# Performance work log

Measured on AMD Instinct MI355X. Metric: run time of the kernel, lower is better.

## Reference

```python
import jax, jax.numpy as jnp
import numpy as np

HIDDEN = 1024
HEADS = 16
HEAD_DIM = HIDDEN // HEADS
B, S = 2, 2048


def setup_inputs() -> dict:
    key = jax.random.key(0)
    ks = jax.random.split(key, 9)
    sc = 1.0 / np.sqrt(HIDDEN)
    return {
        "hidden_state": jax.random.normal(ks[0], (B, S, HIDDEN), dtype=jnp.float32),
        "wq": jax.random.normal(ks[1], (HIDDEN, HIDDEN), dtype=jnp.float32) * sc,
        "bq": jax.random.normal(ks[2], (HIDDEN,), dtype=jnp.float32) * 0.01,
        "wk": jax.random.normal(ks[3], (HIDDEN, HIDDEN), dtype=jnp.float32) * sc,
        "bk": jax.random.normal(ks[4], (HIDDEN,), dtype=jnp.float32) * 0.01,
        "wv": jax.random.normal(ks[5], (HIDDEN, HIDDEN), dtype=jnp.float32) * sc,
        "bv": jax.random.normal(ks[6], (HIDDEN,), dtype=jnp.float32) * 0.01,
        "wo": jax.random.normal(ks[7], (HIDDEN, HIDDEN), dtype=jnp.float32) * sc,
        "bo": jax.random.normal(ks[8], (HIDDEN,), dtype=jnp.float32) * 0.01,
    }


def reference(hidden_state, wq, bq, wk, bk, wv, bv, wo, bo):
    b, s, _ = hidden_state.shape

    def split_head(x):  # [B,S,H*D] -> [B,H,S,D]
        return x.reshape(b, s, HEADS, HEAD_DIM).transpose(0, 2, 1, 3)

    q = split_head(hidden_state @ wq + bq)
    k = split_head(hidden_state @ wk + bk)
    v = split_head(hidden_state @ wv + bv)

    # NOTE: original scales by sqrt(hidden_size), NOT sqrt(head_dim)
    scale = 1.0 / jnp.sqrt(jnp.float32(HIDDEN))
    scores = jnp.einsum("bhqd,bhkd->bhqk", q, k) * scale  # [B,H,S,S]
    probs = jax.nn.softmax(scores, axis=-1)
    out = jnp.einsum("bhqk,bhkd->bhqd", probs, v)  # [B,H,S,D]

    # Faithful to source: transpose(-1,-2) then view (this is the original's
    # layout, which differs from the conventional transpose(1,2) merge)
    out = out.transpose(0, 1, 3, 2).reshape(b, -1, HEADS * HEAD_DIM)
    return out @ wo + bo
```

## Files before the change

### kernel.cpp

```cpp
#include <hip/hip_runtime.h>
#include <stdint.h>


typedef unsigned short u16;
typedef __bf16 bf16x8 __attribute__((ext_vector_type(8)));
typedef u16 u16x8 __attribute__((ext_vector_type(8)));
typedef u16 u16x4 __attribute__((ext_vector_type(4)));
typedef float f32x4 __attribute__((ext_vector_type(4)));

#define DEV static __device__ __forceinline__

DEV bf16x8 as_bf16x8(u16x8 u) { union { u16x8 u; bf16x8 b; } c; c.u = u; return c.b; }
DEV u16 f2bf(float f) {
  uint32_t u = __float_as_uint(f);
  u += 0x7fffu + ((u >> 16) & 1u);
  return (u16)(u >> 16);
}
#if __has_builtin(__builtin_amdgcn_exp2f)
DEV float ex2(float x) { return __builtin_amdgcn_exp2f(x); }
#else
DEV float ex2(float x) { return exp2f(x); }
#endif

DEV void gll16(const u16* g, u16* lds) {
  __builtin_amdgcn_global_load_lds((const __attribute__((address_space(1))) void*)g,
                                   (__attribute__((address_space(3))) void*)lds,
                                   16, 0, 0);
}

__global__ __launch_bounds__(256) void prep_kernel(
    const float* __restrict__ hid, const float* __restrict__ w0,
    const float* __restrict__ w1, const float* __restrict__ w2,
    const float* __restrict__ w3, u16* __restrict__ Ah,
    u16* __restrict__ Wt) {
  __shared__ __align__(16) float T[64][68];
  int bid = blockIdx.x, t = threadIdx.x;
  if (bid < 2048) {
    int i = (bid * 256 + t) * 8;
    f32x4 a = *(const f32x4*)&hid[i];
    f32x4 b = *(const f32x4*)&hid[i + 4];
    u16x8 o;
#pragma unroll
    for (int j = 0; j < 4; ++j) { o[j] = f2bf(a[j]); o[j + 4] = f2bf(b[j]); }
    *(u16x8*)&Ah[i] = o;
    return;
  }
  int tb = bid - 2048;
  int z = tb >> 8, rem = tb & 255;
  const float* W = (z == 0) ? w0 : (z == 1) ? w1 : (z == 2) ? w2 : w3;
  u16* O = Wt + (size_t)z * 1024 * 1024;
  int r0 = (rem >> 4) * 64, c0 = (rem & 15) * 64;
  int i = t >> 2, js = (t & 3) * 16;
#pragma unroll
  for (int jj = 0; jj < 16; jj += 4)
    *(f32x4*)&T[i][js + jj] = *(const f32x4*)&W[(size_t)(r0 + i) * 1024 + c0 + js + jj];
  __syncthreads();
#pragma unroll
  for (int seg = 0; seg < 2; ++seg) {
    u16x8 v;
#pragma unroll
    for (int jj = 0; jj < 8; ++jj) v[jj] = f2bf(T[js + seg * 8 + jj][i]);
    *(u16x8*)&O[(size_t)(c0 + i) * 1024 + r0 + js + seg * 8] = v;
  }
}

DEV void gemm_body(const u16* __restrict__ A, const u16* __restrict__ Bt,
                   const float* __restrict__ bias, u16* __restrict__ C,
                   int mode, float scale) {
  __shared__ __align__(16) u16 As[128 * 32], Bs[128 * 32];
  int tid = threadIdx.x, lane = tid & 63, w = tid >> 6;
  int quad = lane >> 4, l15 = lane & 15;
  int m0 = blockIdx.x * 128, n0 = blockIdx.y * 128;
  int wm = w >> 1, wn = w & 1;
  f32x4 acc[4][4] = {};

  for (int k0 = 0; k0 < 1024; k0 += 32) {
    __syncthreads();
#pragma unroll
    for (int i = 0; i < 2; ++i) {
      int idx = i * 256 + w * 64 + lane;
      int row = idx >> 2, cs = idx & 3, c = cs ^ ((row >> 1) & 3);
      gll16(A + (size_t)(m0 + row) * 1024 + k0 + c * 8, &As[(i * 256 + w * 64) * 8]);
      gll16(Bt + (size_t)(n0 + row) * 1024 + k0 + c * 8, &Bs[(i * 256 + w * 64) * 8]);
    }
    __syncthreads();
    bf16x8 af[4], bfr[4];
#pragma unroll
    for (int mt = 0; mt < 4; ++mt) {
      int row = wm * 64 + mt * 16 + l15;
      af[mt] = as_bf16x8(*(const u16x8*)&As[row * 32 + (quad ^ ((row >> 1) & 3)) * 8]);
    }
#pragma unroll
    for (int nt = 0; nt < 4; ++nt) {
      int row = wn * 64 + nt * 16 + l15;
      bfr[nt] = as_bf16x8(*(const u16x8*)&Bs[row * 32 + (quad ^ ((row >> 1) & 3)) * 8]);
    }
#pragma unroll
    for (int mt = 0; mt < 4; ++mt)
#pragma unroll
      for (int nt = 0; nt < 4; ++nt)
        acc[mt][nt] = __builtin_amdgcn_mfma_f32_16x16x32_bf16(af[mt], bfr[nt], acc[mt][nt], 0, 0, 0);
  }

#pragma unroll
  for (int nt = 0; nt < 4; ++nt) {
    int n = n0 + wn * 64 + nt * 16 + l15;
    float bv = bias[n];
#pragma unroll
    for (int mt = 0; mt < 4; ++mt) {
      int mbase = m0 + wm * 64 + mt * 16 + quad * 4;
      if (mode == 2) {
        int b = mbase >> 11, s = mbase & 2047, h = n >> 6, d = n & 63;
        size_t base = (((size_t)(b * 16 + h)) * 64 + d) * 2048 + s;
        u16x4 pk;
#pragma unroll
        for (int r = 0; r < 4; ++r) pk[r] = f2bf((acc[mt][nt][r] + bv) * scale);
        *(u16x4*)&C[base] = pk;
      } else {
#pragma unroll
        for (int r = 0; r < 4; ++r) {
          int m = mbase + r;
          int b = m >> 11, s = m & 2047, h = n >> 6, d = n & 63;
          C[(((size_t)(b * 16 + h)) * 2048 + s) * 64 + d] =
              f2bf((acc[mt][nt][r] + bv) * scale);
        }
      }
    }
  }
}

__global__ __launch_bounds__(256) void qkv_gemm(
    const u16* __restrict__ A, const u16* __restrict__ Wt,
    const float* __restrict__ bq, const float* __restrict__ bk,
    const float* __restrict__ bv, u16* __restrict__ Qb, u16* __restrict__ Kb,
    u16* __restrict__ Vt) {
  int z = blockIdx.z;
  const u16* Bt = Wt + (size_t)z * 1024 * 1024;
  const float* bias = (z == 0) ? bq : (z == 1) ? bk : bv;
  u16* C = (z == 0) ? Qb : (z == 1) ? Kb : Vt;
  gemm_body(A, Bt, bias, C, (z == 2) ? 2 : 1, (z == 0) ? 0.045084220f : 1.0f);
}

__global__ __launch_bounds__(256) void out_gemm(
    const u16* __restrict__ A, const u16* __restrict__ Wt,
    const float* __restrict__ bo, float* __restrict__ C) {
  const u16* Bt = Wt + (size_t)3 * 1024 * 1024;
  __shared__ __align__(16) u16 As[64 * 32], Bs[128 * 32];
  int tid = threadIdx.x, lane = tid & 63, w = tid >> 6;
  int quad = lane >> 4, l15 = lane & 15;
  int m0 = blockIdx.x * 64, n0 = blockIdx.y * 128;
  f32x4 acc[4][2] = {};

  for (int k0 = 0; k0 < 1024; k0 += 32) {
    __syncthreads();
    {
      int idx = w * 64 + lane;
      int row = idx >> 2, cs = idx & 3, c = cs ^ ((row >> 1) & 3);
      gll16(A + (size_t)(m0 + row) * 1024 + k0 + c * 8, &As[(w * 64) * 8]);
#pragma unroll
      for (int i = 0; i < 2; ++i) {
        int bidx = i * 256 + w * 64 + lane;
        int brow = bidx >> 2, bcs = bidx & 3, bc = bcs ^ ((brow >> 1) & 3);
        gll16(Bt + (size_t)(n0 + brow) * 1024 + k0 + bc * 8,
              &Bs[(i * 256 + w * 64) * 8]);
      }
    }
    __syncthreads();
    bf16x8 af[4], bfr[2];
#pragma unroll
    for (int mt = 0; mt < 4; ++mt) {
      int row = mt * 16 + l15;
      af[mt] = as_bf16x8(*(const u16x8*)&As[row * 32 + (quad ^ ((row >> 1) & 3)) * 8]);
    }
#pragma unroll
    for (int nt = 0; nt < 2; ++nt) {
      int row = w * 32 + nt * 16 + l15;
      bfr[nt] = as_bf16x8(*(const u16x8*)&Bs[row * 32 + (quad ^ ((row >> 1) & 3)) * 8]);
    }
#pragma unroll
    for (int mt = 0; mt < 4; ++mt)
#pragma unroll
      for (int nt = 0; nt < 2; ++nt)
        acc[mt][nt] = __builtin_amdgcn_mfma_f32_16x16x32_bf16(af[mt], bfr[nt], acc[mt][nt], 0, 0, 0);
  }

#pragma unroll
  for (int nt = 0; nt < 2; ++nt) {
    int n = n0 + w * 32 + nt * 16 + l15;
    float bv = bo[n];
#pragma unroll
    for (int mt = 0; mt < 4; ++mt) {
      int mbase = m0 + mt * 16 + quad * 4;
#pragma unroll
      for (int r = 0; r < 4; ++r)
        C[(size_t)(mbase + r) * 1024 + n] = acc[mt][nt][r] + bv;
    }
  }
}

#define PSTR 80
__global__ __launch_bounds__(256, 2) void attn_kernel(
    const u16* __restrict__ Qb, const u16* __restrict__ Kb,
    const u16* __restrict__ Vtb, u16* __restrict__ Otb) {
  __shared__ __align__(16) u16 Ks[2][64 * PSTR], Vs[2][64 * PSTR];
  int tid = threadIdx.x, lane = tid & 63, w = tid >> 6;
  int quad = lane >> 4, l15 = lane & 15;
  int bh = blockIdx.x, q0 = blockIdx.y * 128;
  const size_t baseQK = (size_t)bh * 2048 * 64;

  bf16x8 bq[2][2];
#pragma unroll
  for (int g = 0; g < 2; ++g) {
    int qrow = q0 + w * 32 + g * 16 + l15;
#pragma unroll
    for (int ks = 0; ks < 2; ++ks)
      bq[g][ks] = as_bf16x8(*(const u16x8*)&Qb[baseQK + (size_t)qrow * 64 + (ks * 4 + quad) * 8]);
  }

  bf16x8 av1;
  {
    u16x8 o1;
#pragma unroll
    for (int j = 0; j < 8; ++j) o1[j] = 0x3F80;
    av1 = as_bf16x8(o1);
  }

  f32x4 o[2][4] = {};
  f32x4 l_acc[2] = {};
  const int km = ((l15 & 12) << 1) | (l15 & 3);
  const int srow = tid >> 3, scs = tid & 7;
  const int srow2 = 32 + srow;

  u16x8 tk[2], tv[2];
  tk[0] = *(const u16x8*)&Kb[baseQK + (size_t)srow * 64 + scs * 8];
  tk[1] = *(const u16x8*)&Kb[baseQK + (size_t)srow2 * 64 + scs * 8];
  tv[0] = *(const u16x8*)&Vtb[baseQK + (size_t)srow * 2048 + scs * 8];
  tv[1] = *(const u16x8*)&Vtb[baseQK + (size_t)srow2 * 2048 + scs * 8];
  *(u16x8*)&Ks[0][srow * PSTR + scs * 8] = tk[0];
  *(u16x8*)&Ks[0][srow2 * PSTR + scs * 8] = tk[1];
  *(u16x8*)&Vs[0][srow * PSTR + scs * 8] = tv[0];
  *(u16x8*)&Vs[0][srow2 * PSTR + scs * 8] = tv[1];
  __syncthreads();

  for (int kv = 0; kv < 32; ++kv) {
    int cur = kv & 1;
    if (kv < 31) {
      tk[0] = *(const u16x8*)&Kb[baseQK + (size_t)((kv + 1) * 64 + srow) * 64 + scs * 8];
      tk[1] = *(const u16x8*)&Kb[baseQK + (size_t)((kv + 1) * 64 + srow2) * 64 + scs * 8];
      tv[0] = *(const u16x8*)&Vtb[baseQK + (size_t)srow * 2048 + (kv + 1) * 64 + scs * 8];
      tv[1] = *(const u16x8*)&Vtb[baseQK + (size_t)srow2 * 2048 + (kv + 1) * 64 + scs * 8];
    }

    f32x4 scA[2][2] = {}, scB[2][2] = {};
    __builtin_amdgcn_s_setprio(1);
#pragma unroll
    for (int ks = 0; ks < 2; ++ks)
#pragma unroll
      for (int mtg = 0; mtg < 2; ++mtg) {
        bf16x8 akA = as_bf16x8(*(const u16x8*)&Ks[cur][(mtg * 32 + km) * PSTR + (ks * 4 + quad) * 8]);
        bf16x8 akB = as_bf16x8(*(const u16x8*)&Ks[cur][(mtg * 32 + km + 4) * PSTR + (ks * 4 + quad) * 8]);
#pragma unroll
        for (int g = 0; g < 2; ++g) {
          scA[g][mtg] = __builtin_amdgcn_mfma_f32_16x16x32_bf16(akA, bq[g][ks], scA[g][mtg], 0, 0, 0);
          scB[g][mtg] = __builtin_amdgcn_mfma_f32_16x16x32_bf16(akB, bq[g][ks], scB[g][mtg], 0, 0, 0);
        }
      }
    __builtin_amdgcn_s_setprio(0);

    bf16x8 bp[2][2];
#pragma unroll
    for (int g = 0; g < 2; ++g)
#pragma unroll
      for (int mtg = 0; mtg < 2; ++mtg) {
        float pA0 = ex2(scA[g][mtg][0]), pA1 = ex2(scA[g][mtg][1]);
        float pA2 = ex2(scA[g][mtg][2]), pA3 = ex2(scA[g][mtg][3]);
        float pB0 = ex2(scB[g][mtg][0]), pB1 = ex2(scB[g][mtg][1]);
        float pB2 = ex2(scB[g][mtg][2]), pB3 = ex2(scB[g][mtg][3]);
        bp[g][mtg] = (bf16x8){(__bf16)pA0, (__bf16)pA1, (__bf16)pA2, (__bf16)pA3,
                              (__bf16)pB0, (__bf16)pB1, (__bf16)pB2, (__bf16)pB3};
        l_acc[g] = __builtin_amdgcn_mfma_f32_16x16x32_bf16(av1, bp[g][mtg], l_acc[g], 0, 0, 0);
      }

    __builtin_amdgcn_s_setprio(1);
#pragma unroll
    for (int mtg = 0; mtg < 2; ++mtg)
#pragma unroll
      for (int dt = 0; dt < 4; ++dt) {
        bf16x8 av = as_bf16x8(*(const u16x8*)&Vs[cur][(dt * 16 + l15) * PSTR + (mtg * 4 + quad) * 8]);
#pragma unroll
        for (int g = 0; g < 2; ++g)
          o[g][dt] = __builtin_amdgcn_mfma_f32_16x16x32_bf16(av, bp[g][mtg], o[g][dt], 0, 0, 0);
      }
    __builtin_amdgcn_s_setprio(0);

    if (kv < 31) {
      int nb = cur ^ 1;
      *(u16x8*)&Ks[nb][srow * PSTR + scs * 8] = tk[0];
      *(u16x8*)&Ks[nb][srow2 * PSTR + scs * 8] = tk[1];
      *(u16x8*)&Vs[nb][srow * PSTR + scs * 8] = tv[0];
      *(u16x8*)&Vs[nb][srow2 * PSTR + scs * 8] = tv[1];
    }
    __syncthreads();
  }

#pragma unroll
  for (int g = 0; g < 2; ++g) {
    float inv = 1.0f / l_acc[g][0];
#pragma unroll
    for (int dt = 0; dt < 4; ++dt)
#pragma unroll
      for (int r = 0; r < 4; ++r) {
        int d = dt * 16 + quad * 4 + r;
        Otb[(size_t)bh * 64 * 2048 + (size_t)d * 2048 + q0 + w * 32 + g * 16 + l15] =
            f2bf(o[g][dt][r] * inv);
      }
  }
}

extern "C" void kernel_launch(void* const* d_in, const int* in_sizes, int n_in,
                              void* d_out, int out_size, void* d_ws, size_t ws_size,
                              hipStream_t stream) {
  const float* hid = (const float*)d_in[0];
  const float* wq = (const float*)d_in[1];
  const float* bq = (const float*)d_in[2];
  const float* wk = (const float*)d_in[3];
  const float* bk = (const float*)d_in[4];
  const float* wv = (const float*)d_in[5];
  const float* bv = (const float*)d_in[6];
  const float* wo = (const float*)d_in[7];
  const float* bo = (const float*)d_in[8];

  u16* ws = (u16*)d_ws;
  const size_t MB2 = (size_t)1024 * 1024;
  u16* Wt  = ws;
  u16* Ah  = ws + 4 * MB2;
  u16* Qb  = ws + 8 * MB2;
  u16* Kb  = ws + 12 * MB2;
  u16* Vtb = ws + 16 * MB2;
  u16* Otb = Ah;

  prep_kernel<<<3072, 256, 0, stream>>>(hid, wq, wk, wv, wo, Ah, Wt);
  qkv_gemm<<<dim3(32, 8, 3), 256, 0, stream>>>(Ah, Wt, bq, bk, bv, Qb, Kb, Vtb);
  attn_kernel<<<dim3(32, 16), 256, 0, stream>>>(Qb, Kb, Vtb, Otb);
  out_gemm<<<dim3(64, 8), 256, 0, stream>>>(Otb, Wt, bo, (float*)d_out);
}
```

Before: 181.8 us.

## Split attention KV range across two blocks and add a combine kernel

Splits each attention block's 32 KV tiles into two halves handled by separate blocks (grid z=2). Each half writes its unnormalized partial output in bf16 plus its row sums, and a new combine kernel adds the halves, normalizes and writes the transposed output. This doubles the number of workgroups from 512 to 1024 so more of the GPU's compute units have work. The change also drops LDS double buffering for a single buffer with two barriers per tile, and adds an XOR swizzle on K and a tighter V stride. The costs are an extra launch, extra global traffic for the partials, and an extra bf16 rounding of the partial outputs.

```diff
diff --git a/kernel.cpp b/kernel.cpp
--- a/kernel.cpp
+++ b/kernel.cpp
@@ -16,6 +16,7 @@
   u += 0x7fffu + ((u >> 16) & 1u);
   return (u16)(u >> 16);
 }
+DEV float bf2f(u16 u) { return __uint_as_float((uint32_t)u << 16); }
 #if __has_builtin(__builtin_amdgcn_exp2f)
 DEV float ex2(float x) { return __builtin_amdgcn_exp2f(x); }
 #else
@@ -198,15 +199,19 @@
   }
 }
 
-#define PSTR 80
+#define KSTR 80
+#define VSTR 72
 __global__ __launch_bounds__(256, 2) void attn_kernel(
     const u16* __restrict__ Qb, const u16* __restrict__ Kb,
-    const u16* __restrict__ Vtb, u16* __restrict__ Otb) {
-  __shared__ __align__(16) u16 Ks[2][64 * PSTR], Vs[2][64 * PSTR];
+    const u16* __restrict__ Vtb, u16* __restrict__ opart,
+    float* __restrict__ lpart) {
+  __shared__ __align__(16) u16 Ks[64 * KSTR], Vs[64 * VSTR];
   int tid = threadIdx.x, lane = tid & 63, w = tid >> 6;
   int quad = lane >> 4, l15 = lane & 15;
-  int bh = blockIdx.x, q0 = blockIdx.y * 128;
+  int bh = blockIdx.x, qb = blockIdx.y, z = blockIdx.z;
+  int q0 = qb * 128;
   const size_t baseQK = (size_t)bh * 2048 * 64;
+  const int kvbase = z * 16;
 
   bf16x8 bq[2][2];
 #pragma unroll
@@ -228,23 +233,26 @@
   f32x4 o[2][4] = {};
   f32x4 l_acc[2] = {};
   const int km = ((l15 & 12) << 1) | (l15 & 3);
+  const int swz = l15 >> 2;
   const int srow = tid >> 3, scs = tid & 7;
   const int srow2 = 32 + srow;
+  const int scw = scs ^ (srow >> 3);
 
   u16x8 tk[2], tv[2];
-  tk[0] = *(const u16x8*)&Kb[baseQK + (size_t)srow * 64 + scs * 8];
-  tk[1] = *(const u16x8*)&Kb[baseQK + (size_t)srow2 * 64 + scs * 8];
-  tv[0] = *(const u16x8*)&Vtb[baseQK + (size_t)srow * 2048 + scs * 8];
-  tv[1] = *(const u16x8*)&Vtb[baseQK + (size_t)srow2 * 2048 + scs * 8];
-  *(u16x8*)&Ks[0][srow * PSTR + scs * 8] = tk[0];
-  *(u16x8*)&Ks[0][srow2 * PSTR + scs * 8] = tk[1];
-  *(u16x8*)&Vs[0][srow * PSTR + scs * 8] = tv[0];
-  *(u16x8*)&Vs[0][srow2 * PSTR + scs * 8] = tv[1];
-  __syncthreads();
-
-  for (int kv = 0; kv < 32; ++kv) {
-    int cur = kv & 1;
-    if (kv < 31) {
+  tk[0] = *(const u16x8*)&Kb[baseQK + (size_t)(kvbase * 64 + srow) * 64 + scs * 8];
+  tk[1] = *(const u16x8*)&Kb[baseQK + (size_t)(kvbase * 64 + srow2) * 64 + scs * 8];
+  tv[0] = *(const u16x8*)&Vtb[baseQK + (size_t)srow * 2048 + kvbase * 64 + scs * 8];
+  tv[1] = *(const u16x8*)&Vtb[baseQK + (size_t)srow2 * 2048 + kvbase * 64 + scs * 8];
+
+  for (int kv = kvbase; kv < kvbase + 16; ++kv) {
+    __syncthreads();
+    *(u16x8*)&Ks[srow * KSTR + scw * 8] = tk[0];
+    *(u16x8*)&Ks[srow2 * KSTR + scw * 8] = tk[1];
+    *(u16x8*)&Vs[srow * VSTR + scs * 8] = tv[0];
+    *(u16x8*)&Vs[srow2 * VSTR + scs * 8] = tv[1];
+    __syncthreads();
+
+    if (kv < kvbase + 15) {
       tk[0] = *(const u16x8*)&Kb[baseQK + (size_t)((kv + 1) * 64 + srow) * 64 + scs * 8];
       tk[1] = *(const u16x8*)&Kb[baseQK + (size_t)((kv + 1) * 64 + srow2) * 64 + scs * 8];
       tv[0] = *(const u16x8*)&Vtb[baseQK + (size_t)srow * 2048 + (kv + 1) * 64 + scs * 8];
@@ -257,8 +265,9 @@
     for (int ks = 0; ks < 2; ++ks)
 #pragma unroll
       for (int mtg = 0; mtg < 2; ++mtg) {
-        bf16x8 akA = as_bf16x8(*(const u16x8*)&Ks[cur][(mtg * 32 + km) * PSTR + (ks * 4 + quad) * 8]);
-        bf16x8 akB = as_bf16x8(*(const u16x8*)&Ks[cur][(mtg * 32 + km + 4) * PSTR + (ks * 4 + quad) * 8]);
+        int ck = ((ks * 4 + quad) ^ swz) * 8;
+        bf16x8 akA = as_bf16x8(*(const u16x8*)&Ks[(mtg * 32 + km) * KSTR + ck]);
+        bf16x8 akB = as_bf16x8(*(const u16x8*)&Ks[(mtg * 32 + km + 4) * KSTR + ck]);
 #pragma unroll
         for (int g = 0; g < 2; ++g) {
           scA[g][mtg] = __builtin_amdgcn_mfma_f32_16x16x32_bf16(akA, bq[g][ks], scA[g][mtg], 0, 0, 0);
@@ -286,34 +295,67 @@
     for (int mtg = 0; mtg < 2; ++mtg)
 #pragma unroll
       for (int dt = 0; dt < 4; ++dt) {
-        bf16x8 av = as_bf16x8(*(const u16x8*)&Vs[cur][(dt * 16 + l15) * PSTR + (mtg * 4 + quad) * 8]);
+        bf16x8 av = as_bf16x8(*(const u16x8*)&Vs[(dt * 16 + l15) * VSTR + (mtg * 4 + quad) * 8]);
 #pragma unroll
         for (int g = 0; g < 2; ++g)
           o[g][dt] = __builtin_amdgcn_mfma_f32_16x16x32_bf16(av, bp[g][mtg], o[g][dt], 0, 0, 0);
       }
     __builtin_amdgcn_s_setprio(0);
-
-    if (kv < 31) {
-      int nb = cur ^ 1;
-      *(u16x8*)&Ks[nb][srow * PSTR + scs * 8] = tk[0];
-      *(u16x8*)&Ks[nb][srow2 * PSTR + scs * 8] = tk[1];
-      *(u16x8*)&Vs[nb][srow * PSTR + scs * 8] = tv[0];
-      *(u16x8*)&Vs[nb][srow2 * PSTR + scs * 8] = tv[1];
-    }
-    __syncthreads();
-  }
-
+  }
+
+  int pid = bh * 16 + qb;
+  u16* op = opart + (size_t)(pid * 2 + z) * 128 * 64;
+  float* lp = lpart + (size_t)(pid * 2 + z) * 128;
 #pragma unroll
   for (int g = 0; g < 2; ++g) {
-    float inv = 1.0f / l_acc[g][0];
-#pragma unroll
-    for (int dt = 0; dt < 4; ++dt)
-#pragma unroll
-      for (int r = 0; r < 4; ++r) {
-        int d = dt * 16 + quad * 4 + r;
-        Otb[(size_t)bh * 64 * 2048 + (size_t)d * 2048 + q0 + w * 32 + g * 16 + l15] =
-            f2bf(o[g][dt][r] * inv);
-      }
+    int q = w * 32 + g * 16 + l15;
+    if (quad == 0) lp[q] = l_acc[g][0];
+#pragma unroll
+    for (int dt = 0; dt < 4; ++dt) {
+      u16x4 pk;
+#pragma unroll
+      for (int r = 0; r < 4; ++r) pk[r] = f2bf(o[g][dt][r]);
+      *(u16x4*)&op[q * 64 + dt * 16 + quad * 4] = pk;
+    }
+  }
+}
+
+__global__ __launch_bounds__(256) void attn_combine(
+    const u16* __restrict__ opart, const float* __restrict__ lpart,
+    u16* __restrict__ Otb) {
+  __shared__ float So[128][65];
+  __shared__ float Sl[128];
+  int tid = threadIdx.x, pid = blockIdx.x;
+  int bh = pid >> 4, q0 = (pid & 15) * 128;
+  const u16* o0 = opart + (size_t)pid * 2 * 128 * 64;
+  const u16* o1 = o0 + 128 * 64;
+  const float* l0 = lpart + (size_t)pid * 2 * 128;
+  const float* l1 = l0 + 128;
+  {
+    int q = tid >> 1, dh = (tid & 1) * 32;
+#pragma unroll
+    for (int c = 0; c < 32; c += 8) {
+      u16x8 a = *(const u16x8*)&o0[q * 64 + dh + c];
+      u16x8 b = *(const u16x8*)&o1[q * 64 + dh + c];
+#pragma unroll
+      for (int j = 0; j < 8; ++j)
+        So[q][dh + c + j] = bf2f(a[j]) + bf2f(b[j]);
+    }
+    if (tid < 128) Sl[tid] = 1.0f / (l0[tid] + l1[tid]);
+  }
+  __syncthreads();
+  {
+    int d = tid >> 2, sc = (tid & 3) * 32;
+#pragma unroll
+    for (int c = 0; c < 32; c += 8) {
+      u16x8 ov;
+#pragma unroll
+      for (int j = 0; j < 8; ++j) {
+        int q = sc + c + j;
+        ov[j] = f2bf(So[q][d] * Sl[q]);
+      }
+      *(u16x8*)&Otb[(size_t)bh * 64 * 2048 + (size_t)d * 2048 + q0 + sc + c] = ov;
+    }
   }
 }
 
@@ -338,9 +380,12 @@
   u16* Kb  = ws + 12 * MB2;
   u16* Vtb = ws + 16 * MB2;
   u16* Otb = Ah;
+  u16* opart   = ws + 20 * MB2;
+  float* lpart = (float*)(ws + 28 * MB2);
 
   prep_kernel<<<3072, 256, 0, stream>>>(hid, wq, wk, wv, wo, Ah, Wt);
   qkv_gemm<<<dim3(32, 8, 3), 256, 0, stream>>>(Ah, Wt, bq, bk, bv, Qb, Kb, Vtb);
-  attn_kernel<<<dim3(32, 16), 256, 0, stream>>>(Qb, Kb, Vtb, Otb);
+  attn_kernel<<<dim3(32, 16, 2), 256, 0, stream>>>(Qb, Kb, Vtb, opart, lpart);
+  attn_combine<<<512, 256, 0, stream>>>(opart, lpart, Otb);
   out_gemm<<<dim3(64, 8), 256, 0, stream>>>(Otb, Wt, bo, (float*)d_out);
 }
```

After: 189.5 us. 4.2% more time.

## Double-buffer LDS tiles with register prefetch in QKV and output GEMMs

Applied to the files above, without the earlier changes.

Both projection GEMMs move from direct global-to-LDS loads with two barriers per k-step to a double-buffered LDS scheme. The next k-tile is prefetched into registers before the MFMA block and written to the other LDS buffer afterwards, leaving one barrier per iteration. MFMA sections are wrapped in s_setprio raises. This aims to hide global load latency behind compute, at the cost of doubled LDS use, extra registers, and a trip through VGPRs instead of the direct LDS load path.

```diff
diff --git a/kernel.cpp b/kernel.cpp
--- a/kernel.cpp
+++ b/kernel.cpp
@@ -67,39 +67,68 @@
 DEV void gemm_body(const u16* __restrict__ A, const u16* __restrict__ Bt,
                    const float* __restrict__ bias, u16* __restrict__ C,
                    int mode, float scale) {
-  __shared__ __align__(16) u16 As[128 * 32], Bs[128 * 32];
+  __shared__ __align__(16) u16 As[2][128 * 32], Bs[2][128 * 32];
   int tid = threadIdx.x, lane = tid & 63, w = tid >> 6;
   int quad = lane >> 4, l15 = lane & 15;
   int m0 = blockIdx.x * 128, n0 = blockIdx.y * 128;
   int wm = w >> 1, wn = w & 1;
   f32x4 acc[4][4] = {};
 
+  const int idx0 = tid, idx1 = 256 + tid;
+  const int row0 = idx0 >> 2, c0g = ((idx0 & 3) ^ ((row0 >> 1) & 3)) * 8;
+  const int row1 = idx1 >> 2, c1g = ((idx1 & 3) ^ ((row1 >> 1) & 3)) * 8;
+  const u16* Ap0 = A + (size_t)(m0 + row0) * 1024 + c0g;
+  const u16* Ap1 = A + (size_t)(m0 + row1) * 1024 + c1g;
+  const u16* Bp0 = Bt + (size_t)(n0 + row0) * 1024 + c0g;
+  const u16* Bp1 = Bt + (size_t)(n0 + row1) * 1024 + c1g;
+
+  u16x8 ta0, ta1, tb0, tb1;
+  ta0 = *(const u16x8*)Ap0;
+  ta1 = *(const u16x8*)Ap1;
+  tb0 = *(const u16x8*)Bp0;
+  tb1 = *(const u16x8*)Bp1;
+  *(u16x8*)&As[0][idx0 * 8] = ta0;
+  *(u16x8*)&As[0][idx1 * 8] = ta1;
+  *(u16x8*)&Bs[0][idx0 * 8] = tb0;
+  *(u16x8*)&Bs[0][idx1 * 8] = tb1;
+  __syncthreads();
+
   for (int k0 = 0; k0 < 1024; k0 += 32) {
-    __syncthreads();
-#pragma unroll
-    for (int i = 0; i < 2; ++i) {
-      int idx = i * 256 + w * 64 + lane;
-      int row = idx >> 2, cs = idx & 3, c = cs ^ ((row >> 1) & 3);
-      gll16(A + (size_t)(m0 + row) * 1024 + k0 + c * 8, &As[(i * 256 + w * 64) * 8]);
-      gll16(Bt + (size_t)(n0 + row) * 1024 + k0 + c * 8, &Bs[(i * 256 + w * 64) * 8]);
-    }
-    __syncthreads();
+    int cur = (k0 >> 5) & 1;
+    if (k0 < 992) {
+      ta0 = *(const u16x8*)(Ap0 + k0 + 32);
+      ta1 = *(const u16x8*)(Ap1 + k0 + 32);
+      tb0 = *(const u16x8*)(Bp0 + k0 + 32);
+      tb1 = *(const u16x8*)(Bp1 + k0 + 32);
+    }
+
     bf16x8 af[4], bfr[4];
 #pragma unroll
     for (int mt = 0; mt < 4; ++mt) {
       int row = wm * 64 + mt * 16 + l15;
-      af[mt] = as_bf16x8(*(const u16x8*)&As[row * 32 + (quad ^ ((row >> 1) & 3)) * 8]);
+      af[mt] = as_bf16x8(*(const u16x8*)&As[cur][row * 32 + (quad ^ ((row >> 1) & 3)) * 8]);
     }
 #pragma unroll
     for (int nt = 0; nt < 4; ++nt) {
       int row = wn * 64 + nt * 16 + l15;
-      bfr[nt] = as_bf16x8(*(const u16x8*)&Bs[row * 32 + (quad ^ ((row >> 1) & 3)) * 8]);
-    }
+      bfr[nt] = as_bf16x8(*(const u16x8*)&Bs[cur][row * 32 + (quad ^ ((row >> 1) & 3)) * 8]);
+    }
+    __builtin_amdgcn_s_setprio(1);
 #pragma unroll
     for (int mt = 0; mt < 4; ++mt)
 #pragma unroll
       for (int nt = 0; nt < 4; ++nt)
         acc[mt][nt] = __builtin_amdgcn_mfma_f32_16x16x32_bf16(af[mt], bfr[nt], acc[mt][nt], 0, 0, 0);
+    __builtin_amdgcn_s_setprio(0);
+
+    if (k0 < 992) {
+      int nb = cur ^ 1;
+      *(u16x8*)&As[nb][idx0 * 8] = ta0;
+      *(u16x8*)&As[nb][idx1 * 8] = ta1;
+      *(u16x8*)&Bs[nb][idx0 * 8] = tb0;
+      *(u16x8*)&Bs[nb][idx1 * 8] = tb1;
+    }
+    __syncthreads();
   }
 
 #pragma unroll
@@ -145,43 +174,63 @@
     const u16* __restrict__ A, const u16* __restrict__ Wt,
     const float* __restrict__ bo, float* __restrict__ C) {
   const u16* Bt = Wt + (size_t)3 * 1024 * 1024;
-  __shared__ __align__(16) u16 As[64 * 32], Bs[128 * 32];
+  __shared__ __align__(16) u16 As[2][64 * 32], Bs[2][128 * 32];
   int tid = threadIdx.x, lane = tid & 63, w = tid >> 6;
   int quad = lane >> 4, l15 = lane & 15;
   int m0 = blockIdx.x * 64, n0 = blockIdx.y * 128;
   f32x4 acc[4][2] = {};
 
+  const int arow = tid >> 2, acg = ((tid & 3) ^ ((arow >> 1) & 3)) * 8;
+  const int bidx0 = tid, bidx1 = 256 + tid;
+  const int brow0 = bidx0 >> 2, bc0 = ((bidx0 & 3) ^ ((brow0 >> 1) & 3)) * 8;
+  const int brow1 = bidx1 >> 2, bc1 = ((bidx1 & 3) ^ ((brow1 >> 1) & 3)) * 8;
+  const u16* Ap = A + (size_t)(m0 + arow) * 1024 + acg;
+  const u16* Bp0 = Bt + (size_t)(n0 + brow0) * 1024 + bc0;
+  const u16* Bp1 = Bt + (size_t)(n0 + brow1) * 1024 + bc1;
+
+  u16x8 ta, tb0, tb1;
+  ta = *(const u16x8*)Ap;
+  tb0 = *(const u16x8*)Bp0;
+  tb1 = *(const u16x8*)Bp1;
+  *(u16x8*)&As[0][tid * 8] = ta;
+  *(u16x8*)&Bs[0][bidx0 * 8] = tb0;
+  *(u16x8*)&Bs[0][bidx1 * 8] = tb1;
+  __syncthreads();
+
   for (int k0 = 0; k0 < 1024; k0 += 32) {
-    __syncthreads();
-    {
-      int idx = w * 64 + lane;
-      int row = idx >> 2, cs = idx & 3, c = cs ^ ((row >> 1) & 3);
-      gll16(A + (size_t)(m0 + row) * 1024 + k0 + c * 8, &As[(w * 64) * 8]);
-#pragma unroll
-      for (int i = 0; i < 2; ++i) {
-        int bidx = i * 256 + w * 64 + lane;
-        int brow = bidx >> 2, bcs = bidx & 3, bc = bcs ^ ((brow >> 1) & 3);
-        gll16(Bt + (size_t)(n0 + brow) * 1024 + k0 + bc * 8,
-              &Bs[(i * 256 + w * 64) * 8]);
-      }
-    }
-    __syncthreads();
+    int cur = (k0 >> 5) & 1;
+    if (k0 < 992) {
+      ta = *(const u16x8*)(Ap + k0 + 32);
+      tb0 = *(const u16x8*)(Bp0 + k0 + 32);
+      tb1 = *(const u16x8*)(Bp1 + k0 + 32);
+    }
+
     bf16x8 af[4], bfr[2];
 #pragma unroll
     for (int mt = 0; mt < 4; ++mt) {
       int row = mt * 16 + l15;
-      af[mt] = as_bf16x8(*(const u16x8*)&As[row * 32 + (quad ^ ((row >> 1) & 3)) * 8]);
+      af[mt] = as_bf16x8(*(const u16x8*)&As[cur][row * 32 + (quad ^ ((row >> 1) & 3)) * 8]);
     }
 #pragma unroll
     for (int nt = 0; nt < 2; ++nt) {
       int row = w * 32 + nt * 16 + l15;
-      bfr[nt] = as_bf16x8(*(const u16x8*)&Bs[row * 32 + (quad ^ ((row >> 1) & 3)) * 8]);
-    }
+      bfr[nt] = as_bf16x8(*(const u16x8*)&Bs[cur][row * 32 + (quad ^ ((row >> 1) & 3)) * 8]);
+    }
+    __builtin_amdgcn_s_setprio(1);
 #pragma unroll
     for (int mt = 0; mt < 4; ++mt)
 #pragma unroll
       for (int nt = 0; nt < 2; ++nt)
         acc[mt][nt] = __builtin_amdgcn_mfma_f32_16x16x32_bf16(af[mt], bfr[nt], acc[mt][nt], 0, 0, 0);
+    __builtin_amdgcn_s_setprio(0);
+
+    if (k0 < 992) {
+      int nb = cur ^ 1;
+      *(u16x8*)&As[nb][tid * 8] = ta;
+      *(u16x8*)&Bs[nb][bidx0 * 8] = tb0;
+      *(u16x8*)&Bs[nb][bidx1 * 8] = tb1;
+    }
+    __syncthreads();
   }
 
 #pragma unroll
```

New measurement: 179.6 us. About the same (-1.2%).
